# Optimization experiments

Measured on AMD Instinct MI355X. Metric: run time of the kernel, lower is better.

## Reference

```python
import jax, jax.numpy as jnp
import numpy as np

D_MODEL = 256
N = 8192

def setup_inputs() -> dict:
    key = jax.random.key(0)
    k1, k2, k3, k4 = jax.random.split(key, 4)
    x = jax.random.normal(k1, (N, D_MODEL), dtype=jnp.float32)
    # nn.Linear weights: shape [out, in], applied as x @ W.T
    s = 1.0 / np.sqrt(D_MODEL)
    Wq = jax.random.normal(k2, (D_MODEL, D_MODEL), dtype=jnp.float32) * s
    Wk = jax.random.normal(k3, (D_MODEL, D_MODEL), dtype=jnp.float32) * s
    Wv = jax.random.normal(k4, (D_MODEL, D_MODEL), dtype=jnp.float32) * s
    return {"x": x, "Wq": Wq, "Wk": Wk, "Wv": Wv}

def reference(x, Wq, Wk, Wv):
    d_model = Wq.shape[0]
    Q = x @ Wq.T  # [N, d]
    K = x @ Wk.T
    V = x @ Wv.T
    scores = (Q @ K.T) / jnp.sqrt(jnp.asarray(d_model, x.dtype))  # [N, N]
    attn = jax.nn.softmax(scores, axis=-1)  # stable max-sub softmax, same math
    cntx = attn @ V  # [N, d]
    return (cntx, attn)
```

## Files before the change

### kernel.cpp

```cpp
#include <hip/hip_runtime.h>

#define D_MODEL 256
#define NSEQ    8192
#define PV_GROUPS 8

typedef _Float16 half8 __attribute__((ext_vector_type(8)));
typedef _Float16 half4 __attribute__((ext_vector_type(4)));
typedef float    f32x4 __attribute__((ext_vector_type(4)));

__device__ __forceinline__ half8 cvt8(f32x4 a, f32x4 b) {
  half8 h;
  h[0]=(_Float16)a[0]; h[1]=(_Float16)a[1]; h[2]=(_Float16)a[2]; h[3]=(_Float16)a[3];
  h[4]=(_Float16)b[0]; h[5]=(_Float16)b[1]; h[6]=(_Float16)b[2]; h[7]=(_Float16)b[3];
  return h;
}

__device__ __forceinline__ half8 load8_f32(const float* p) {
  f32x4 a = *(const f32x4*)p;
  f32x4 b = *(const f32x4*)(p + 4);
  return cvt8(a, b);
}

__global__ __launch_bounds__(256) void qkv_kernel(
    const float* __restrict__ x, const float* __restrict__ Wq,
    const float* __restrict__ Wk, const float* __restrict__ Wv,
    _Float16* __restrict__ QK16, _Float16* __restrict__ VT)
{
  const int tid  = threadIdx.x;
  const int lane = tid & 63;
  const int wave = tid >> 6;
  const int c    = lane & 15;
  const int quad = lane >> 4;
  const int M0   = blockIdx.x * 128 + (wave >> 1) * 64;
  const int Nblk = blockIdx.y * 128 + (wave & 1) * 64;
  const int widx = Nblk >> 8;
  const int nloc = Nblk & 255;
  const float* W = (widx == 0) ? Wq : (widx == 1 ? Wk : Wv);

  f32x4 acc[4][4] = {};
  for (int k0 = 0; k0 < D_MODEL; k0 += 32) {
    half8 af[4], bf[4];
#pragma unroll
    for (int mt = 0; mt < 4; ++mt)
      af[mt] = load8_f32(&x[(size_t)(M0 + mt*16 + c) * D_MODEL + k0 + quad*8]);
#pragma unroll
    for (int nt = 0; nt < 4; ++nt)
      bf[nt] = load8_f32(&W[(size_t)(nloc + nt*16 + c) * D_MODEL + k0 + quad*8]);
#pragma unroll
    for (int mt = 0; mt < 4; ++mt)
#pragma unroll
      for (int nt = 0; nt < 4; ++nt)
        acc[mt][nt] = __builtin_amdgcn_mfma_f32_16x16x32_f16(af[mt], bf[nt], acc[mt][nt], 0, 0, 0);
  }

  if (widx < 2) {
#pragma unroll
    for (int mt = 0; mt < 4; ++mt)
#pragma unroll
      for (int nt = 0; nt < 4; ++nt) {
        const int col  = widx * 256 + nloc + nt*16 + c;
        const int row0 = M0 + mt*16 + quad*4;
#pragma unroll
        for (int r = 0; r < 4; ++r)
          QK16[(size_t)(row0 + r) * 512 + col] = (_Float16)acc[mt][nt][r];
      }
  } else {
#pragma unroll
    for (int mt = 0; mt < 4; ++mt)
#pragma unroll
      for (int nt = 0; nt < 4; ++nt) {
        const int d  = nloc + nt*16 + c;
        const int m0 = M0 + mt*16 + quad*4;
        half4 h;
        h[0]=(_Float16)acc[mt][nt][0]; h[1]=(_Float16)acc[mt][nt][1];
        h[2]=(_Float16)acc[mt][nt][2]; h[3]=(_Float16)acc[mt][nt][3];
        *(half4*)&VT[(size_t)d * NSEQ + m0] = h;
      }
  }
}

template<bool P16>
__global__ __launch_bounds__(256) void score_kernel(
    const _Float16* __restrict__ QK16, void* __restrict__ Pout,
    float* __restrict__ lsum)
{
  const int tid  = threadIdx.x;
  const int lane = tid & 63;
  const int wave = tid >> 6;
  const int c    = lane & 15;
  const int quad = lane >> 4;
  const int M0   = blockIdx.x * 128 + (wave >> 1) * 64;
  const int N0   = blockIdx.y * 128 + (wave & 1) * 64;

  f32x4 acc[4][4] = {};
  for (int k0 = 0; k0 < 256; k0 += 32) {
    half8 af[4], bf[4];
#pragma unroll
    for (int mt = 0; mt < 4; ++mt)
      af[mt] = *(const half8*)&QK16[(size_t)(M0 + mt*16 + c) * 512 + k0 + quad*8];
#pragma unroll
    for (int nt = 0; nt < 4; ++nt)
      bf[nt] = *(const half8*)&QK16[(size_t)(N0 + nt*16 + c) * 512 + 256 + k0 + quad*8];
#pragma unroll
    for (int mt = 0; mt < 4; ++mt)
#pragma unroll
      for (int nt = 0; nt < 4; ++nt)
        acc[mt][nt] = __builtin_amdgcn_mfma_f32_16x16x32_f16(af[mt], bf[nt], acc[mt][nt], 0, 0, 0);
  }

  float psum[4][4] = {};
#pragma unroll
  for (int mt = 0; mt < 4; ++mt)
#pragma unroll
    for (int nt = 0; nt < 4; ++nt)
#pragma unroll
      for (int r = 0; r < 4; ++r) {
        const float p = __expf(acc[mt][nt][r] * 0.0625f);
        psum[mt][r] += p;
        const size_t idx = (size_t)(M0 + mt*16 + quad*4 + r) * NSEQ + N0 + nt*16 + c;
        if constexpr (P16) ((_Float16*)Pout)[idx] = (_Float16)p;
        else               ((float*)Pout)[idx]    = p;
      }

#pragma unroll
  for (int mt = 0; mt < 4; ++mt)
#pragma unroll
    for (int r = 0; r < 4; ++r) {
      float v = psum[mt][r];
      v += __shfl_xor(v, 1);
      v += __shfl_xor(v, 2);
      v += __shfl_xor(v, 4);
      v += __shfl_xor(v, 8);
      if (c == 0) atomicAdd(&lsum[M0 + mt*16 + quad*4 + r], v);
    }
}

template<bool P16>
__global__ __launch_bounds__(256) void pv_kernel(
    const void* __restrict__ Pin, float* __restrict__ attn,
    const float* __restrict__ lsum, const _Float16* __restrict__ VT,
    float* __restrict__ cntx)
{
  __shared__ float linv[32];
  const int tid  = threadIdx.x;
  const int lane = tid & 63;
  const int wave = tid >> 6;
  const int c    = lane & 15;
  const int quad = lane >> 4;
  const int M0   = blockIdx.x * 32;
  const int jb   = blockIdx.y * (NSEQ / PV_GROUPS);
  const int je   = jb + NSEQ / PV_GROUPS;
  const int D0   = wave * 64;
  const int nr   = tid >> 3;
  const int ncol = (tid & 7) * 8;

  if (tid < 32) linv[tid] = 1.0f / lsum[M0 + tid];
  __syncthreads();
  const float nscale = linv[nr];

  f32x4 acc[2][4] = {};
  for (int j0 = jb; j0 < je; j0 += 64) {
    half8 np16; f32x4 np0, np1;
    if constexpr (P16) {
      np16 = *(const half8*)((const _Float16*)Pin + (size_t)(M0 + nr) * NSEQ + j0 + ncol);
    } else {
      const float* pr = (const float*)Pin + (size_t)(M0 + nr) * NSEQ + j0 + ncol;
      np0 = *(const f32x4*)pr; np1 = *(const f32x4*)(pr + 4);
    }

    half8 af[2][2], bf[4][2];
#pragma unroll
    for (int h = 0; h < 2; ++h) {
#pragma unroll
      for (int mt = 0; mt < 2; ++mt) {
        if constexpr (P16) {
          af[mt][h] = *(const half8*)((const _Float16*)Pin +
                        (size_t)(M0 + mt*16 + c) * NSEQ + j0 + h*32 + quad*8);
        } else {
          const float* pa = (const float*)Pin +
                        (size_t)(M0 + mt*16 + c) * NSEQ + j0 + h*32 + quad*8;
          af[mt][h] = cvt8(*(const f32x4*)pa, *(const f32x4*)(pa + 4));
        }
      }
#pragma unroll
      for (int nt = 0; nt < 4; ++nt)
        bf[nt][h] = *(const half8*)&VT[(size_t)(D0 + nt*16 + c) * NSEQ + j0 + h*32 + quad*8];
    }

    if constexpr (!P16) __syncthreads();

    {
      float* ar = attn + (size_t)(M0 + nr) * NSEQ + j0 + ncol;
      f32x4 w0, w1;
      if constexpr (P16) {
#pragma unroll
        for (int r = 0; r < 4; ++r) {
          w0[r] = (float)np16[r]     * nscale;
          w1[r] = (float)np16[r + 4] * nscale;
        }
      } else {
        w0 = np0 * nscale; w1 = np1 * nscale;
      }
      *(f32x4*)ar       = w0;
      *(f32x4*)(ar + 4) = w1;
    }

#pragma unroll
    for (int h = 0; h < 2; ++h)
#pragma unroll
      for (int mt = 0; mt < 2; ++mt)
#pragma unroll
        for (int nt = 0; nt < 4; ++nt)
          acc[mt][nt] = __builtin_amdgcn_mfma_f32_16x16x32_f16(af[mt][h], bf[nt][h], acc[mt][nt], 0, 0, 0);
  }

#pragma unroll
  for (int mt = 0; mt < 2; ++mt)
#pragma unroll
    for (int r = 0; r < 4; ++r) {
      const float s = linv[mt*16 + quad*4 + r];
#pragma unroll
      for (int nt = 0; nt < 4; ++nt)
        atomicAdd(&cntx[(size_t)(M0 + mt*16 + quad*4 + r) * D_MODEL + D0 + nt*16 + c],
                  acc[mt][nt][r] * s);
    }
}

extern "C" void kernel_launch(void* const* d_in, const int* in_sizes, int n_in,
                              void* d_out, int out_size, void* d_ws, size_t ws_size,
                              hipStream_t stream)
{
  const float* x  = (const float*)d_in[0];
  const float* Wq = (const float*)d_in[1];
  const float* Wk = (const float*)d_in[2];
  const float* Wv = (const float*)d_in[3];

  float* cntx = (float*)d_out;
  float* attn = cntx + (size_t)NSEQ * D_MODEL;

  _Float16* QK16 = (_Float16*)d_ws;
  _Float16* VT   = QK16 + (size_t)NSEQ * 512;
  float*    lsum = (float*)(VT + (size_t)D_MODEL * NSEQ);
  _Float16* P16  = (_Float16*)(lsum + NSEQ);

  const size_t base_bytes = (size_t)NSEQ*512*2 + (size_t)D_MODEL*NSEQ*2 + (size_t)NSEQ*4;
  const bool big_ws = ws_size >= base_bytes + (size_t)NSEQ * NSEQ * 2;

  hipMemsetAsync(cntx, 0, sizeof(float) * (size_t)NSEQ * D_MODEL, stream);
  hipMemsetAsync(lsum, 0, sizeof(float) * NSEQ, stream);

  qkv_kernel<<<dim3(64, 6), 256, 0, stream>>>(x, Wq, Wk, Wv, QK16, VT);

  if (big_ws) {
    score_kernel<true><<<dim3(64, 64), 256, 0, stream>>>(QK16, (void*)P16, lsum);
    pv_kernel<true><<<dim3(NSEQ/32, PV_GROUPS), 256, 0, stream>>>(
        (const void*)P16, attn, lsum, VT, cntx);
  } else {
    score_kernel<false><<<dim3(64, 64), 256, 0, stream>>>(QK16, (void*)attn, lsum);
    pv_kernel<false><<<dim3(NSEQ/32, PV_GROUPS), 256, 0, stream>>>(
        (const void*)attn, attn, lsum, VT, cntx);
  }
}
```

Measured before the change: 656.4 us.

## Double-buffer register loads in score and PV kernels, split QKV into single-wave blocks

The score and fp16 PV kernels now prefetch the next K-step's fragments into a second register set while the MFMAs for the current step run, overlapping global load latency with compute. Launch bounds ask for 3 blocks per SIMD, which caps registers. The QKV projection now uses one wave per block over a 128x12 grid so there are more, smaller blocks. Doubling the fragment registers under a tighter register cap risks spilling.

Measured after the change: 642.2 us. 2.2% less time.

```diff
diff --git a/kernel.cpp b/kernel.cpp
--- a/kernel.cpp
+++ b/kernel.cpp
@@ -21,18 +21,16 @@
   return cvt8(a, b);
 }
 
-__global__ __launch_bounds__(256) void qkv_kernel(
+__global__ __launch_bounds__(64, 3) void qkv_kernel(
     const float* __restrict__ x, const float* __restrict__ Wq,
     const float* __restrict__ Wk, const float* __restrict__ Wv,
     _Float16* __restrict__ QK16, _Float16* __restrict__ VT)
 {
-  const int tid  = threadIdx.x;
-  const int lane = tid & 63;
-  const int wave = tid >> 6;
+  const int lane = threadIdx.x & 63;
   const int c    = lane & 15;
   const int quad = lane >> 4;
-  const int M0   = blockIdx.x * 128 + (wave >> 1) * 64;
-  const int Nblk = blockIdx.y * 128 + (wave & 1) * 64;
+  const int M0   = blockIdx.x * 64;
+  const int Nblk = blockIdx.y * 64;
   const int widx = Nblk >> 8;
   const int nloc = Nblk & 255;
   const float* W = (widx == 0) ? Wq : (widx == 1 ? Wk : Wv);
@@ -80,7 +78,7 @@
 }
 
 template<bool P16>
-__global__ __launch_bounds__(256) void score_kernel(
+__global__ __launch_bounds__(256, 3) void score_kernel(
     const _Float16* __restrict__ QK16, void* __restrict__ Pout,
     float* __restrict__ lsum)
 {
@@ -93,19 +91,31 @@
   const int N0   = blockIdx.y * 128 + (wave & 1) * 64;
 
   f32x4 acc[4][4] = {};
-  for (int k0 = 0; k0 < 256; k0 += 32) {
-    half8 af[4], bf[4];
+  half8 afA[4], bfA[4], afB[4], bfB[4];
+
+  auto ld = [&](half8 (&af)[4], half8 (&bf)[4], int k0) {
 #pragma unroll
     for (int mt = 0; mt < 4; ++mt)
       af[mt] = *(const half8*)&QK16[(size_t)(M0 + mt*16 + c) * 512 + k0 + quad*8];
 #pragma unroll
     for (int nt = 0; nt < 4; ++nt)
       bf[nt] = *(const half8*)&QK16[(size_t)(N0 + nt*16 + c) * 512 + 256 + k0 + quad*8];
+  };
+  auto mm = [&](half8 (&af)[4], half8 (&bf)[4]) {
 #pragma unroll
     for (int mt = 0; mt < 4; ++mt)
 #pragma unroll
       for (int nt = 0; nt < 4; ++nt)
         acc[mt][nt] = __builtin_amdgcn_mfma_f32_16x16x32_f16(af[mt], bf[nt], acc[mt][nt], 0, 0, 0);
+  };
+
+  ld(afA, bfA, 0);
+#pragma unroll
+  for (int k0 = 0; k0 < 256; k0 += 64) {
+    ld(afB, bfB, k0 + 32);
+    mm(afA, bfA);
+    if (k0 + 64 < 256) ld(afA, bfA, k0 + 64);
+    mm(afB, bfB);
   }
 
   float psum[4][4] = {};
@@ -135,9 +145,8 @@
     }
 }
 
-template<bool P16>
-__global__ __launch_bounds__(256) void pv_kernel(
-    const void* __restrict__ Pin, float* __restrict__ attn,
+__global__ __launch_bounds__(256, 3) void pv_kernel_p16(
+    const _Float16* __restrict__ P16, float* __restrict__ attn,
     const float* __restrict__ lsum, const _Float16* __restrict__ VT,
     float* __restrict__ cntx)
 {
@@ -159,51 +168,106 @@
   const float nscale = linv[nr];
 
   f32x4 acc[2][4] = {};
+  half8 afA[2][2], bfA[4][2], npA;
+  half8 afB[2][2], bfB[4][2], npB;
+
+  auto ld = [&](half8 (&af)[2][2], half8 (&bf)[4][2], half8& np, int j0) {
+    np = *(const half8*)&P16[(size_t)(M0 + nr) * NSEQ + j0 + ncol];
+#pragma unroll
+    for (int h = 0; h < 2; ++h) {
+#pragma unroll
+      for (int mt = 0; mt < 2; ++mt)
+        af[mt][h] = *(const half8*)&P16[(size_t)(M0 + mt*16 + c) * NSEQ + j0 + h*32 + quad*8];
+#pragma unroll
+      for (int nt = 0; nt < 4; ++nt)
+        bf[nt][h] = *(const half8*)&VT[(size_t)(D0 + nt*16 + c) * NSEQ + j0 + h*32 + quad*8];
+    }
+  };
+  auto consume = [&](half8 (&af)[2][2], half8 (&bf)[4][2], half8& np, int j0) {
+    f32x4 w0, w1;
+#pragma unroll
+    for (int r = 0; r < 4; ++r) {
+      w0[r] = (float)np[r]     * nscale;
+      w1[r] = (float)np[r + 4] * nscale;
+    }
+    float* ar = attn + (size_t)(M0 + nr) * NSEQ + j0 + ncol;
+    *(f32x4*)ar       = w0;
+    *(f32x4*)(ar + 4) = w1;
+#pragma unroll
+    for (int h = 0; h < 2; ++h)
+#pragma unroll
+      for (int mt = 0; mt < 2; ++mt)
+#pragma unroll
+        for (int nt = 0; nt < 4; ++nt)
+          acc[mt][nt] = __builtin_amdgcn_mfma_f32_16x16x32_f16(af[mt][h], bf[nt][h], acc[mt][nt], 0, 0, 0);
+  };
+
+  ld(afA, bfA, npA, jb);
+  for (int j0 = jb; j0 < je; j0 += 128) {
+    ld(afB, bfB, npB, j0 + 64);
+    consume(afA, bfA, npA, j0);
+    if (j0 + 128 < je) ld(afA, bfA, npA, j0 + 128);
+    consume(afB, bfB, npB, j0 + 64);
+  }
+
+#pragma unroll
+  for (int mt = 0; mt < 2; ++mt)
+#pragma unroll
+    for (int r = 0; r < 4; ++r) {
+      const float s = linv[mt*16 + quad*4 + r];
+#pragma unroll
+      for (int nt = 0; nt < 4; ++nt)
+        atomicAdd(&cntx[(size_t)(M0 + mt*16 + quad*4 + r) * D_MODEL + D0 + nt*16 + c],
+                  acc[mt][nt][r] * s);
+    }
+}
+
+__global__ __launch_bounds__(256) void pv_kernel_f32(
+    const float* __restrict__ Pin, float* __restrict__ attn,
+    const float* __restrict__ lsum, const _Float16* __restrict__ VT,
+    float* __restrict__ cntx)
+{
+  __shared__ float linv[32];
+  const int tid  = threadIdx.x;
+  const int lane = tid & 63;
+  const int wave = tid >> 6;
+  const int c    = lane & 15;
+  const int quad = lane >> 4;
+  const int M0   = blockIdx.x * 32;
+  const int jb   = blockIdx.y * (NSEQ / PV_GROUPS);
+  const int je   = jb + NSEQ / PV_GROUPS;
+  const int D0   = wave * 64;
+  const int nr   = tid >> 3;
+  const int ncol = (tid & 7) * 8;
+
+  if (tid < 32) linv[tid] = 1.0f / lsum[M0 + tid];
+  __syncthreads();
+  const float nscale = linv[nr];
+
+  f32x4 acc[2][4] = {};
   for (int j0 = jb; j0 < je; j0 += 64) {
-    half8 np16; f32x4 np0, np1;
-    if constexpr (P16) {
-      np16 = *(const half8*)((const _Float16*)Pin + (size_t)(M0 + nr) * NSEQ + j0 + ncol);
-    } else {
-      const float* pr = (const float*)Pin + (size_t)(M0 + nr) * NSEQ + j0 + ncol;
-      np0 = *(const f32x4*)pr; np1 = *(const f32x4*)(pr + 4);
-    }
+    const float* pr = Pin + (size_t)(M0 + nr) * NSEQ + j0 + ncol;
+    f32x4 np0 = *(const f32x4*)pr;
+    f32x4 np1 = *(const f32x4*)(pr + 4);
 
     half8 af[2][2], bf[4][2];
 #pragma unroll
     for (int h = 0; h < 2; ++h) {
 #pragma unroll
       for (int mt = 0; mt < 2; ++mt) {
-        if constexpr (P16) {
-          af[mt][h] = *(const half8*)((const _Float16*)Pin +
-                        (size_t)(M0 + mt*16 + c) * NSEQ + j0 + h*32 + quad*8);
-        } else {
-          const float* pa = (const float*)Pin +
-                        (size_t)(M0 + mt*16 + c) * NSEQ + j0 + h*32 + quad*8;
-          af[mt][h] = cvt8(*(const f32x4*)pa, *(const f32x4*)(pa + 4));
-        }
+        const float* pa = Pin + (size_t)(M0 + mt*16 + c) * NSEQ + j0 + h*32 + quad*8;
+        af[mt][h] = cvt8(*(const f32x4*)pa, *(const f32x4*)(pa + 4));
       }
 #pragma unroll
       for (int nt = 0; nt < 4; ++nt)
         bf[nt][h] = *(const half8*)&VT[(size_t)(D0 + nt*16 + c) * NSEQ + j0 + h*32 + quad*8];
     }
 
-    if constexpr (!P16) __syncthreads();
-
-    {
-      float* ar = attn + (size_t)(M0 + nr) * NSEQ + j0 + ncol;
-      f32x4 w0, w1;
-      if constexpr (P16) {
-#pragma unroll
-        for (int r = 0; r < 4; ++r) {
-          w0[r] = (float)np16[r]     * nscale;
-          w1[r] = (float)np16[r + 4] * nscale;
-        }
-      } else {
-        w0 = np0 * nscale; w1 = np1 * nscale;
-      }
-      *(f32x4*)ar       = w0;
-      *(f32x4*)(ar + 4) = w1;
-    }
+    __syncthreads();
+
+    float* ar = attn + (size_t)(M0 + nr) * NSEQ + j0 + ncol;
+    *(f32x4*)ar       = np0 * nscale;
+    *(f32x4*)(ar + 4) = np1 * nscale;
 
 #pragma unroll
     for (int h = 0; h < 2; ++h)
@@ -249,15 +313,13 @@
   hipMemsetAsync(cntx, 0, sizeof(float) * (size_t)NSEQ * D_MODEL, stream);
   hipMemsetAsync(lsum, 0, sizeof(float) * NSEQ, stream);
 
-  qkv_kernel<<<dim3(64, 6), 256, 0, stream>>>(x, Wq, Wk, Wv, QK16, VT);
+  qkv_kernel<<<dim3(128, 12), 64, 0, stream>>>(x, Wq, Wk, Wv, QK16, VT);
 
   if (big_ws) {
     score_kernel<true><<<dim3(64, 64), 256, 0, stream>>>(QK16, (void*)P16, lsum);
-    pv_kernel<true><<<dim3(NSEQ/32, PV_GROUPS), 256, 0, stream>>>(
-        (const void*)P16, attn, lsum, VT, cntx);
+    pv_kernel_p16<<<dim3(NSEQ/32, PV_GROUPS), 256, 0, stream>>>(P16, attn, lsum, VT, cntx);
   } else {
     score_kernel<false><<<dim3(64, 64), 256, 0, stream>>>(QK16, (void*)attn, lsum);
-    pv_kernel<false><<<dim3(NSEQ/32, PV_GROUPS), 256, 0, stream>>>(
-        (const void*)attn, attn, lsum, VT, cntx);
-  }
-}
+    pv_kernel_f32<<<dim3(NSEQ/32, PV_GROUPS), 256, 0, stream>>>(attn, attn, lsum, VT, cntx);
+  }
+}
```
